# Optimization experiments

Hardware: AMD Instinct MI355X
Metric: run time of the kernel (lower is better)

## Reference

```python
import jax, jax.numpy as jnp
import numpy as np

D_MODEL = 768
NUM_HEADS = 12
D_K = D_MODEL // NUM_HEADS
D_FF = 3072
EPS = 1e-5


def _layer_norm(x, gamma, beta):
    mu = jnp.mean(x, axis=-1, keepdims=True)
    var = jnp.mean(jnp.square(x - mu), axis=-1, keepdims=True)
    return (x - mu) * jax.lax.rsqrt(var + EPS) * gamma + beta


def setup_inputs() -> dict:
    key = jax.random.key(0)
    ks = jax.random.split(key, 16)
    s = 1.0 / np.sqrt(D_MODEL)
    sf = 1.0 / np.sqrt(D_FF)
    inp = {
        "x": jax.random.normal(ks[0], (2, 2048, D_MODEL), dtype=jnp.float32),
        "Wq": jax.random.uniform(ks[1], (D_MODEL, D_MODEL), jnp.float32, -s, s),
        "bq": jax.random.uniform(ks[2], (D_MODEL,), jnp.float32, -s, s),
        "Wk": jax.random.uniform(ks[3], (D_MODEL, D_MODEL), jnp.float32, -s, s),
        "bk": jax.random.uniform(ks[4], (D_MODEL,), jnp.float32, -s, s),
        "Wv": jax.random.uniform(ks[5], (D_MODEL, D_MODEL), jnp.float32, -s, s),
        "bv": jax.random.uniform(ks[6], (D_MODEL,), jnp.float32, -s, s),
        "Wo": jax.random.uniform(ks[7], (D_MODEL, D_MODEL), jnp.float32, -s, s),
        "bo": jax.random.uniform(ks[8], (D_MODEL,), jnp.float32, -s, s),
        "W1": jax.random.uniform(ks[9], (D_MODEL, D_FF), jnp.float32, -s, s),
        "b1": jax.random.uniform(ks[10], (D_FF,), jnp.float32, -s, s),
        "W2": jax.random.uniform(ks[11], (D_FF, D_MODEL), jnp.float32, -sf, sf),
        "b2": jax.random.uniform(ks[12], (D_MODEL,), jnp.float32, -sf, sf),
        "g1": jnp.ones((D_MODEL,), jnp.float32),
        "be1": jnp.zeros((D_MODEL,), jnp.float32),
        "g2": jnp.ones((D_MODEL,), jnp.float32),
        "be2": jnp.zeros((D_MODEL,), jnp.float32),
    }
    return inp


def reference(x, Wq, bq, Wk, bk, Wv, bv, Wo, bo, W1, b1, W2, b2, g1, be1, g2, be2):
    B, S, _ = x.shape

    def split(h):  # (B,S,D) -> (B,H,S,Dk)
        return h.reshape(B, S, NUM_HEADS, D_K).transpose(0, 2, 1, 3)

    q = split(x @ Wq + bq)
    k = split(x @ Wk + bk)
    v = split(x @ Wv + bv)

    # naive attention: materialize full (B,H,S,S) scores as in the original
    scores = jnp.einsum("bhsd,bhtd->bhst", q, k) / np.sqrt(D_K)
    attn = jax.nn.softmax(scores, axis=-1)
    ctx = jnp.einsum("bhst,bhtd->bhsd", attn, v)
    ctx = ctx.transpose(0, 2, 1, 3).reshape(B, S, D_MODEL)
    attn_out = ctx @ Wo + bo

    x = _layer_norm(x + attn_out, g1, be1)
    ff = jax.nn.relu(x @ W1 + b1) @ W2 + b2
    x = _layer_norm(x + ff, g2, be2)
    return x
```

## Files before the change

kernel.cpp:

```cpp
#include <hip/hip_runtime.h>
#include <cstdint>


typedef unsigned short u16;
typedef unsigned int u32;
typedef __attribute__((ext_vector_type(4))) float f32x4;
typedef __attribute__((ext_vector_type(8))) short s16x8;
typedef __attribute__((ext_vector_type(4))) u16  u16x4;
typedef __attribute__((ext_vector_type(2))) u32  u32x2;

#define AS1 __attribute__((address_space(1)))
#define AS3 __attribute__((address_space(3)))

__device__ __forceinline__ u16 f2b(float f) {
  union { float f; unsigned u; } v; v.f = f;
  unsigned r = v.u + 0x7FFFu + ((v.u >> 16) & 1u);
  return (u16)(r >> 16);
}

__device__ __forceinline__ float b2f(u16 v) {
  union { float f; u32 u; } x; x.u = ((u32)v) << 16; return x.f;
}

__device__ __forceinline__ void gl_lds16(const void* g, void* lds_uniform_base) {
  __builtin_amdgcn_global_load_lds((const AS1 void*)g, (AS3 void*)lds_uniform_base, 16, 0, 0);
}

__device__ __forceinline__ f32x4 mfma16(s16x8 a, s16x8 b, f32x4 c) {
  return __builtin_amdgcn_mfma_f32_16x16x32_bf16(a, b, c, 0, 0, 0);
}

__device__ __forceinline__ u32 cvt_pk_bf16(float lo, float hi) {
  u32 r;
  asm("v_cvt_pk_bf16_f32 %0, %1, %2" : "=v"(r) : "v"(lo), "v"(hi));
  return r;
}

__device__ __forceinline__ float max3f(float a, float b, float c) {
  return fmaxf(fmaxf(a, b), c);
}

__device__ __forceinline__ void block_barrier() {
  asm volatile("" ::: "memory");
  __builtin_amdgcn_s_barrier();
  asm volatile("" ::: "memory");
}

__global__ __launch_bounds__(256) void prep(
    const float* __restrict__ Wq, const float* __restrict__ Wk,
    const float* __restrict__ Wv, const float* __restrict__ Wo,
    const float* __restrict__ W1, const float* __restrict__ W2,
    const float* __restrict__ bq, const float* __restrict__ bk,
    const float* __restrict__ bv, const float* __restrict__ x,
    u16* __restrict__ Wqkv_t, u16* __restrict__ Wo_t,
    u16* __restrict__ W1_t, u16* __restrict__ W2_t,
    float* __restrict__ bqkv, u16* __restrict__ Xb, int convBlocks) {
  __shared__ float ts[32][33];
  const int bid = blockIdx.x;
  const int tx = threadIdx.x, ty = threadIdx.y;
  if (bid < 6912) {
    const float* W; u16* Wt; int K, N, tile;
    if (bid < 2304) {
      int w = bid / 576; tile = bid - w * 576; K = 768; N = 768;
      W = (w == 0) ? Wq : (w == 1) ? Wk : (w == 2) ? Wv : Wo;
      Wt = (w < 3) ? Wqkv_t + (size_t)w * 768 * 768 : Wo_t;
    } else if (bid < 4608) {
      tile = bid - 2304; K = 768; N = 3072; W = W1; Wt = W1_t;
    } else {
      tile = bid - 4608; K = 3072; N = 768; W = W2; Wt = W2_t;
    }
    int ntx = N >> 5;
    int n0 = (tile % ntx) * 32, k0 = (tile / ntx) * 32;
#pragma unroll
    for (int yy = 0; yy < 32; yy += 8)
      ts[ty + yy][tx] = W[(size_t)(k0 + ty + yy) * N + n0 + tx];
    __syncthreads();
#pragma unroll
    for (int yy = 0; yy < 32; yy += 8)
      Wt[(size_t)(n0 + ty + yy) * K + k0 + tx] = f2b(ts[tx][ty + yy]);
  } else if (bid < 6912 + convBlocks) {
    int t = ty * 32 + tx;
    size_t i = ((size_t)(bid - 6912) * 256 + t) * 4;
    f32x4 v = *(const f32x4*)(x + i);
    u16x4 o;
#pragma unroll
    for (int k = 0; k < 4; ++k) o[k] = f2b(v[k]);
    *(u16x4*)(Xb + i) = o;
  } else {
    int t = ty * 32 + tx;
    int i = (bid - 6912 - convBlocks) * 256 + t;
    if (i < 2304) bqkv[i] = (i < 768) ? bq[i] : (i < 1536) ? bk[i - 768] : bv[i - 1536];
  }
}

template <int MODE>
__global__ __launch_bounds__(256) void gemm_bt(const u16* __restrict__ A,
                                               const u16* __restrict__ Bt,
                                               const float* __restrict__ bias,
                                               u16* __restrict__ Cb,
                                               u16* __restrict__ Qo, u16* __restrict__ Ko,
                                               u16* __restrict__ Vt, int M, int N, int K,
                                               int Klen) {
  __shared__ __align__(16) u16 lsA[2][128 * 64];
  __shared__ __align__(16) u16 lsB[2][128 * 64];
  const int tid = threadIdx.x;
  const int lane = tid & 63, wave = tid >> 6;
  const int lr = lane & 15, lh = lane >> 4;
  const int wr = wave >> 1, wc = wave & 1;

  int bx, by, bz;
  {
    int nx = gridDim.x, ny = gridDim.y, nz = gridDim.z;
    int total = nx * ny * nz;
    int lin = blockIdx.x + nx * (blockIdx.y + ny * blockIdx.z);
    if ((total & 7) == 0) {
      int key = (lin & 7) * (total >> 3) + (lin >> 3);
      by = key % ny;
      int t2 = key / ny;
      bz = t2 % nz;
      bx = t2 / nz;
    } else {
      bx = blockIdx.x; by = blockIdx.y; bz = blockIdx.z;
    }
  }
  const int m0 = by * 128;
  const int n0 = bx * 128;
  const int kB = bz * Klen;

  f32x4 acc[4][4];
#pragma unroll
  for (int i = 0; i < 4; ++i)
#pragma unroll
    for (int j = 0; j < 4; ++j) acc[i][j] = f32x4{0.f, 0.f, 0.f, 0.f};

  const size_t aBase = (size_t)m0 * K;
  const size_t bBase = (size_t)n0 * K;
  const int srow8 = tid >> 3;
  const int scolE = (((tid & 7) * 16) ^ ((srow8 & 7) << 4)) >> 1;
  const int xk = (lr & 7) << 4;

  auto stage = [&](int buf, int kt) {
#pragma unroll
    for (int i = 0; i < 4; ++i) {
      int row = i * 32 + srow8;
      int ldsOff = buf * 16384 + i * 4096 + wave * 1024;
      gl_lds16(A + aBase + (size_t)row * K + kt + scolE, (char*)lsA + ldsOff);
      gl_lds16(Bt + bBase + (size_t)row * K + kt + scolE, (char*)lsB + ldsOff);
    }
  };

  const int nk = Klen >> 6;
  stage(0, kB);
  for (int t = 0; t < nk; ++t) {
    const int cur = t & 1;
    if (t + 1 < nk) {
      stage(cur ^ 1, kB + (t + 1) * 64);
      asm volatile("s_waitcnt vmcnt(8)" ::: "memory");
    } else {
      asm volatile("s_waitcnt vmcnt(0)" ::: "memory");
    }
    block_barrier();
    const char* baA = (const char*)lsA + cur * 16384;
    const char* baB = (const char*)lsB + cur * 16384;
#pragma unroll
    for (int ks = 0; ks < 2; ++ks) {
      int cb = (ks * 64 + lh * 16) ^ xk;
      s16x8 a[4], b[4];
#pragma unroll
      for (int i = 0; i < 4; ++i) {
        a[i] = *(const s16x8*)(baA + (wr * 64 + i * 16 + lr) * 128 + cb);
        b[i] = *(const s16x8*)(baB + (wc * 64 + i * 16 + lr) * 128 + cb);
      }
#pragma unroll
      for (int i = 0; i < 4; ++i)
#pragma unroll
        for (int j = 0; j < 4; ++j) acc[i][j] = mfma16(a[i], b[j], acc[i][j]);
    }
    block_barrier();
  }

  u16* CbP = Cb + (size_t)bz * M * N;
#pragma unroll
  for (int i = 0; i < 4; ++i) {
    int growb = m0 + wr * 64 + i * 16 + lh * 4;
#pragma unroll
    for (int j = 0; j < 4; ++j) {
      int col = n0 + wc * 64 + j * 16 + lr;
      float bv = (MODE != 0 || bz == 0) ? bias[col] : 0.f;
      if (MODE == 2) {
        int sel = col / 768;
        int c2 = col - sel * 768;
        int h = c2 >> 6, d = c2 & 63;
        int b = growb >> 11, s0 = growb & 2047;
        if (sel == 2) {
          u16x4 ob;
#pragma unroll
          for (int q = 0; q < 4; ++q) ob[q] = f2b(acc[i][j][q] + bv);
          *(u16x4*)(Vt + (((size_t)(b * 12 + h)) * 64 + d) * 2048 + s0) = ob;
        } else {
#pragma unroll
          for (int q = 0; q < 4; ++q) {
            float v = acc[i][j][q] + bv;
            size_t idx = (((size_t)(b * 12 + h)) * 2048 + (s0 + q)) * 64 + d;
            float vv = (sel == 0) ? v * 0.1803368801f : v;
            u16* dst = (sel == 0) ? Qo : Ko;
            dst[idx] = f2b(vv);
          }
        }
      } else {
#pragma unroll
        for (int q = 0; q < 4; ++q) {
          int grow = growb + q;
          float v = acc[i][j][q] + bv;
          if (MODE == 0) {
            CbP[(size_t)grow * N + col] = f2b(v);
          } else {
            Cb[(size_t)grow * N + col] = f2b(fmaxf(v, 0.f));
          }
        }
      }
    }
  }
}

__global__ __launch_bounds__(512) void attn(const u16* __restrict__ Qh,
                                            const u16* __restrict__ Kh,
                                            const u16* __restrict__ Vt,
                                            u16* __restrict__ Opb,
                                            float* __restrict__ ml,
                                            int nbh, int ntile) {
  __shared__ __align__(16) u16 lsK[2][64 * 64];
  __shared__ __align__(16) u16 lsV[2][64 * 64];
  __shared__ __align__(16) u16 lsP[8][16 * 64];
  const int tid = threadIdx.x, lane = tid & 63, wave = tid >> 6;
  const int lr = lane & 15, lh = lane >> 4;

  int bx = blockIdx.x, bh = blockIdx.y, z = blockIdx.z;
  {
    int nz = gridDim.z;
    int total = 16 * nbh * nz;
    if ((total & 7) == 0) {
      int lin = bx + 16 * (bh + nbh * z);
      int nl = (lin & 7) * (total >> 3) + (lin >> 3);
      bx = nl & 15;
      bh = (nl >> 4) % nbh;
      z = nl / (16 * nbh);
    }
  }
  const int q0 = bx * 128 + wave * 16;
  const size_t kvBase = (size_t)bh * 2048 * 64;
  const int tB = z * ntile;

  const int srow = tid >> 3;
  const int scol = (((tid & 7) * 16) ^ ((srow & 7) << 4)) >> 1;
  const u16* kSrcBase = Kh + kvBase + (size_t)srow * 64 + scol;
  const u16* vSrcBase = Vt + kvBase + (size_t)srow * 2048 + scol;

  s16x8 qf[2];
#pragma unroll
  for (int ks = 0; ks < 2; ++ks)
    qf[ks] = *(const s16x8*)(Qh + kvBase + (size_t)(q0 + lr) * 64 + ks * 32 + lh * 8);

  s16x8 onesf;
#pragma unroll
  for (int k = 0; k < 8; ++k) onesf[k] = (short)0x3F80;

  f32x4 oacc[4];
  f32x4 aOnes = f32x4{0.f, 0.f, 0.f, 0.f};
  float mrow = -1e30f;
#pragma unroll
  for (int d = 0; d < 4; ++d) oacc[d] = f32x4{0.f, 0.f, 0.f, 0.f};

  gl_lds16(kSrcBase + (size_t)tB * 4096, (char*)lsK[0] + wave * 1024);
  gl_lds16(vSrcBase + tB * 64,           (char*)lsV[0] + wave * 1024);

  for (int it = 0; it < ntile; ++it) {
    const int cur = it & 1;
    __syncthreads();

    s16x8 kb[2][4];
#pragma unroll
    for (int ks = 0; ks < 2; ++ks)
#pragma unroll
      for (int j = 0; j < 4; ++j) {
        int r = j * 16 + lr;
        kb[ks][j] = *(const s16x8*)((const char*)lsK[cur] + r * 128 +
                                    ((ks * 64 + lh * 16) ^ ((r & 7) << 4)));
      }

    if (it + 1 < ntile) {
      int t = tB + it + 1;
      gl_lds16(kSrcBase + (size_t)t * 4096, (char*)lsK[cur ^ 1] + wave * 1024);
      gl_lds16(vSrcBase + t * 64,           (char*)lsV[cur ^ 1] + wave * 1024);
    }

    f32x4 st[4];
#pragma unroll
    for (int j = 0; j < 4; ++j) st[j] = f32x4{0.f, 0.f, 0.f, 0.f};
    __builtin_amdgcn_s_setprio(1);
#pragma unroll
    for (int ks = 0; ks < 2; ++ks)
#pragma unroll
      for (int j = 0; j < 4; ++j) st[j] = mfma16(kb[ks][j], qf[ks], st[j]);
    __builtin_amdgcn_s_setprio(0);

    float mx;
    {
      float t0 = max3f(st[0][0], st[0][1], st[0][2]);
      float t1 = max3f(st[0][3], st[1][0], st[1][1]);
      float t2 = max3f(st[1][2], st[1][3], st[2][0]);
      float t3 = max3f(st[2][1], st[2][2], st[2][3]);
      float t4 = max3f(st[3][0], st[3][1], st[3][2]);
      mx = fmaxf(max3f(t0, t1, t2), max3f(t3, t4, st[3][3]));
      mx = fmaxf(mx, __shfl_xor(mx, 16));
      mx = fmaxf(mx, __shfl_xor(mx, 32));
    }
    if (__any(mx > mrow + 11.f)) {
      float mn = fmaxf(mrow, mx);
      float al = exp2f(mrow - mn);
      mrow = mn;
#pragma unroll
      for (int q = 0; q < 4; ++q) aOnes[q] *= al;
#pragma unroll
      for (int d = 0; d < 4; ++d)
#pragma unroll
        for (int q = 0; q < 4; ++q) oacc[d][q] *= al;
    }

#pragma unroll
    for (int j = 0; j < 4; ++j) {
      float p0 = exp2f(st[j][0] - mrow);
      float p1 = exp2f(st[j][1] - mrow);
      float p2 = exp2f(st[j][2] - mrow);
      float p3 = exp2f(st[j][3] - mrow);
      u32x2 pk;
      pk.x = cvt_pk_bf16(p0, p1);
      pk.y = cvt_pk_bf16(p2, p3);
      *(u32x2*)((char*)lsP[wave] + lr * 128 + ((j * 32 + lh * 8) ^ ((lr & 7) << 4))) = pk;
    }

    __builtin_amdgcn_s_setprio(1);
#pragma unroll
    for (int ks = 0; ks < 2; ++ks) {
      s16x8 pa = *(const s16x8*)((const char*)lsP[wave] + lr * 128 +
                                 ((ks * 64 + lh * 16) ^ ((lr & 7) << 4)));
      aOnes = mfma16(onesf, pa, aOnes);
#pragma unroll
      for (int d = 0; d < 4; ++d) {
        int r = d * 16 + lr;
        s16x8 vb = *(const s16x8*)((const char*)lsV[cur] + r * 128 +
                                   ((ks * 64 + lh * 16) ^ ((r & 7) << 4)));
        oacc[d] = mfma16(vb, pa, oacc[d]);
      }
    }
    __builtin_amdgcn_s_setprio(0);
  }

  {
    int s = q0 + lr;
    size_t r = ((size_t)z * nbh + bh) * 2048 + s;
#pragma unroll
    for (int d = 0; d < 4; ++d) {
      u32x2 pk;
      pk.x = cvt_pk_bf16(oacc[d][0], oacc[d][1]);
      pk.y = cvt_pk_bf16(oacc[d][2], oacc[d][3]);
      *(u32x2*)(Opb + r * 64 + d * 16 + lh * 4) = pk;
    }
    if (lh == 0) { ml[r * 2] = mrow; ml[r * 2 + 1] = aOnes[0]; }
  }
}

template <int NZ>
__global__ __launch_bounds__(256) void attn_combine(const u16* __restrict__ Opb,
                                                    const float* __restrict__ ml,
                                                    u16* __restrict__ ctx, int nbh) {
  size_t i = (size_t)blockIdx.x * 256 + threadIdx.x;
  int d4 = (int)(i & 15);
  size_t rs = i >> 4;
  size_t zs = (size_t)nbh * 2048;
  float m[NZ], l[NZ];
  float mx = -1e30f;
#pragma unroll
  for (int p = 0; p < NZ; ++p) {
    m[p] = ml[(p * zs + rs) * 2];
    l[p] = ml[(p * zs + rs) * 2 + 1];
    mx = fmaxf(mx, m[p]);
  }
  float wsum = 0.f, a[NZ];
#pragma unroll
  for (int p = 0; p < NZ; ++p) { a[p] = exp2f(m[p] - mx); wsum += l[p] * a[p]; }
  float inv = 1.f / wsum;
  f32x4 o = f32x4{0.f, 0.f, 0.f, 0.f};
#pragma unroll
  for (int p = 0; p < NZ; ++p) {
    u16x4 op = *(const u16x4*)(Opb + (p * zs + rs) * 64 + d4 * 4);
#pragma unroll
    for (int k = 0; k < 4; ++k) o[k] += b2f(op[k]) * a[p];
  }
  int bh = (int)(rs >> 11), s = (int)(rs & 2047);
  int b = bh / 12, h = bh - b * 12;
  u16x4 r;
#pragma unroll
  for (int k = 0; k < 4; ++k) r[k] = f2b(o[k] * inv);
  *(u16x4*)(ctx + ((size_t)(b * 2048 + s)) * 768 + h * 64 + d4 * 4) = r;
}

template <int NP>
__global__ __launch_bounds__(256) void resid_ln(const float* __restrict__ xin,
                                                const u16* __restrict__ yp,
                                                size_t pstride,
                                                const float* __restrict__ gamma,
                                                const float* __restrict__ beta,
                                                float* __restrict__ outf,
                                                u16* __restrict__ outb) {
  const int row = blockIdx.x, t = threadIdx.x;
  const size_t base4 = (size_t)row * 192;
  const bool act = t < 192;
  f32x4 v = f32x4{0.f, 0.f, 0.f, 0.f};
  float s = 0.f, s2 = 0.f;
  if (act) {
    v = ((const f32x4*)xin)[base4 + t];
#pragma unroll
    for (int p = 0; p < NP; ++p) {
      u16x4 y = *(const u16x4*)(yp + p * pstride + (size_t)row * 768 + t * 4);
#pragma unroll
      for (int k = 0; k < 4; ++k) v[k] += b2f(y[k]);
    }
    s = (v[0] + v[1]) + (v[2] + v[3]);
    s2 = (v[0] * v[0] + v[1] * v[1]) + (v[2] * v[2] + v[3] * v[3]);
  }
#pragma unroll
  for (int off = 32; off > 0; off >>= 1) {
    s += __shfl_down(s, off, 64);
    s2 += __shfl_down(s2, off, 64);
  }
  __shared__ float red[8];
  int lane = t & 63, wave = t >> 6;
  if (lane == 0) { red[wave] = s; red[4 + wave] = s2; }
  __syncthreads();
  s = red[0] + red[1] + red[2] + red[3];
  s2 = red[4] + red[5] + red[6] + red[7];
  const float inv = 1.f / 768.f;
  float mu = s * inv;
  float var = fmaxf(s2 * inv - mu * mu, 0.f);
  float rs = rsqrtf(var + 1e-5f);
  if (act) {
    f32x4 g = ((const f32x4*)gamma)[t];
    f32x4 bb = ((const f32x4*)beta)[t];
    f32x4 o;
#pragma unroll
    for (int k = 0; k < 4; ++k) o[k] = (v[k] - mu) * rs * g[k] + bb[k];
    if (outf) ((f32x4*)outf)[base4 + t] = o;
    if (outb) {
      u16x4 ob;
#pragma unroll
      for (int k = 0; k < 4; ++k) ob[k] = f2b(o[k]);
      ((u16x4*)outb)[base4 + t] = ob;
    }
  }
}

extern "C" void kernel_launch(void* const* d_in, const int* in_sizes, int n_in,
                              void* d_out, int out_size, void* d_ws, size_t ws_size,
                              hipStream_t stream) {
  const float* x   = (const float*)d_in[0];
  const float* Wq  = (const float*)d_in[1];
  const float* bq  = (const float*)d_in[2];
  const float* Wk  = (const float*)d_in[3];
  const float* bk  = (const float*)d_in[4];
  const float* Wv  = (const float*)d_in[5];
  const float* bv  = (const float*)d_in[6];
  const float* Wo  = (const float*)d_in[7];
  const float* bo  = (const float*)d_in[8];
  const float* W1  = (const float*)d_in[9];
  const float* b1  = (const float*)d_in[10];
  const float* W2  = (const float*)d_in[11];
  const float* b2  = (const float*)d_in[12];
  const float* g1  = (const float*)d_in[13];
  const float* be1 = (const float*)d_in[14];
  const float* g2  = (const float*)d_in[15];
  const float* be2 = (const float*)d_in[16];
  float* out = (float*)d_out;

  const int M = in_sizes[0] / 768;
  const int B = M / 2048;
  const int nbh = B * 12;

  char* ws = (char*)d_ws;
  size_t off = 0;
  auto alloc = [&](size_t bytes) -> void* {
    void* p = ws + off;
    off += (bytes + 255) & ~(size_t)255;
    return p;
  };
  u16*   Wqkv_t = (u16*)alloc((size_t)2304 * 768 * 2);
  u16*   Wo_t   = (u16*)alloc((size_t)768 * 768 * 2);
  u16*   W1_t   = (u16*)alloc((size_t)3072 * 768 * 2);
  u16*   W2_t   = (u16*)alloc((size_t)768 * 3072 * 2);
  float* bqkv   = (float*)alloc(2304 * 4);
  u16*   Xb     = (u16*)alloc((size_t)M * 768 * 2);
  u16*   Qh     = (u16*)alloc((size_t)M * 768 * 2);
  u16*   Kh     = (u16*)alloc((size_t)M * 768 * 2);
  u16*   Vt     = (u16*)alloc((size_t)M * 768 * 2);

  size_t pstride = (size_t)M * 768;
  size_t fixedRest = pstride * 4  + pstride * 2  +
                     (size_t)M * 3072 * 2  + 4096;
  const int ZSPLIT = 2;
  size_t opElems = (size_t)ZSPLIT * nbh * 2048 * 64;
  size_t attnBytes = opElems * 2 + (size_t)ZSPLIT * nbh * 2048 * 2 * 4;
  size_t reg4 = attnBytes;
  if (reg4 < pstride * 2 * 4) reg4 = pstride * 2 * 4;
  int FSPLIT;
  size_t regionBytes;
  if (off + reg4 + fixedRest <= ws_size) {
    FSPLIT = 4; regionBytes = reg4;
  } else {
    FSPLIT = 2;
    regionBytes = attnBytes > pstride * 2 * 2 ? attnBytes : pstride * 2 * 2;
  }
  float* region = (float*)alloc(regionBytes);
  u16*   Opb  = (u16*)region;
  float* ml   = (float*)((char*)region + opElems * 2);
  u16*   projPart = (u16*)region;
  u16*   ffnPart  = (u16*)region;
  float* x1f  = (float*)alloc(pstride * 4);
  u16*   x1b  = (u16*)alloc(pstride * 2);
  u16*   hb   = (u16*)alloc((size_t)M * 3072 * 2);
  u16*   ctx  = Xb;

  dim3 tb(32, 8);
  const int convBlocks = (M * 768) / 1024;
  prep<<<6912 + convBlocks + 9, tb, 0, stream>>>(
      Wq, Wk, Wv, Wo, W1, W2, bq, bk, bv, x,
      Wqkv_t, Wo_t, W1_t, W2_t, bqkv, Xb, convBlocks);

  gemm_bt<2><<<dim3(2304 / 128, M / 128), 256, 0, stream>>>(
      Xb, Wqkv_t, bqkv, nullptr, Qh, Kh, Vt, M, 2304, 768, 768);

  attn<<<dim3(16, nbh, ZSPLIT), 512, 0, stream>>>(Qh, Kh, Vt, Opb, ml, nbh, 32 / ZSPLIT);
  attn_combine<2><<<nbh * 128, 256, 0, stream>>>(Opb, ml, ctx, nbh);

  gemm_bt<0><<<dim3(768 / 128, M / 128, 2), 256, 0, stream>>>(
      ctx, Wo_t, bo, projPart, nullptr, nullptr, nullptr, M, 768, 768, 384);

  resid_ln<2><<<M, 256, 0, stream>>>(x, projPart, pstride, g1, be1, x1f, x1b);

  gemm_bt<1><<<dim3(3072 / 128, M / 128), 256, 0, stream>>>(
      x1b, W1_t, b1, hb, nullptr, nullptr, nullptr, M, 3072, 768, 768);

  if (FSPLIT == 4) {
    gemm_bt<0><<<dim3(768 / 128, M / 128, 4), 256, 0, stream>>>(
        hb, W2_t, b2, ffnPart, nullptr, nullptr, nullptr, M, 768, 3072, 768);
    resid_ln<4><<<M, 256, 0, stream>>>(x1f, ffnPart, pstride, g2, be2, out, nullptr);
  } else {
    gemm_bt<0><<<dim3(768 / 128, M / 128, 2), 256, 0, stream>>>(
        hb, W2_t, b2, ffnPart, nullptr, nullptr, nullptr, M, 768, 3072, 1536);
    resid_ln<2><<<M, 256, 0, stream>>>(x1f, ffnPart, pstride, g2, be2, out, nullptr);
  }
}
```

Measured before the change: 202.5 us.

## Single-buffer attention K/V via register prefetch and fold max subtraction into MFMA init

Replaces the double-buffered direct global-to-LDS K/V loads with a register-staged prefetch into a single LDS buffer, which halves K/V shared memory but adds a second barrier per tile. The running max is now subtracted by seeding the score accumulators with -mrow, so the exp no longer needs a per-element subtraction except on rescale tiles. This aims to raise occupancy and remove VALU subtractions, at the cost of extra register pressure and synchronisation.

New measurement: 210.2 us. 1.04x slower.

```diff
diff --git a/kernel.cpp b/kernel.cpp
--- a/kernel.cpp
+++ b/kernel.cpp
@@ -229,8 +229,8 @@
                                             u16* __restrict__ Opb,
                                             float* __restrict__ ml,
                                             int nbh, int ntile) {
-  __shared__ __align__(16) u16 lsK[2][64 * 64];
-  __shared__ __align__(16) u16 lsV[2][64 * 64];
+  __shared__ __align__(16) u16 lsK[64 * 64];
+  __shared__ __align__(16) u16 lsV[64 * 64];
   __shared__ __align__(16) u16 lsP[8][16 * 64];
   const int tid = threadIdx.x, lane = tid & 63, wave = tid >> 6;
   const int lr = lane & 15, lh = lane >> 4;
@@ -267,16 +267,23 @@
 
   f32x4 oacc[4];
   f32x4 aOnes = f32x4{0.f, 0.f, 0.f, 0.f};
-  float mrow = -1e30f;
+  float mrow = 0.f;
 #pragma unroll
   for (int d = 0; d < 4; ++d) oacc[d] = f32x4{0.f, 0.f, 0.f, 0.f};
 
-  gl_lds16(kSrcBase + (size_t)tB * 4096, (char*)lsK[0] + wave * 1024);
-  gl_lds16(vSrcBase + tB * 64,           (char*)lsV[0] + wave * 1024);
+  s16x8 kr = *(const s16x8*)(kSrcBase + (size_t)tB * 4096);
+  s16x8 vr = *(const s16x8*)(vSrcBase + tB * 64);
+  *(s16x8*)((char*)lsK + tid * 16) = kr;
+  *(s16x8*)((char*)lsV + tid * 16) = vr;
+  __syncthreads();
 
   for (int it = 0; it < ntile; ++it) {
-    const int cur = it & 1;
-    __syncthreads();
+    const bool more = (it + 1 < ntile);
+    if (more) {
+      int t = tB + it + 1;
+      kr = *(const s16x8*)(kSrcBase + (size_t)t * 4096);
+      vr = *(const s16x8*)(vSrcBase + t * 64);
+    }
 
     s16x8 kb[2][4];
 #pragma unroll
@@ -284,19 +291,14 @@
 #pragma unroll
       for (int j = 0; j < 4; ++j) {
         int r = j * 16 + lr;
-        kb[ks][j] = *(const s16x8*)((const char*)lsK[cur] + r * 128 +
+        kb[ks][j] = *(const s16x8*)((const char*)lsK + r * 128 +
                                     ((ks * 64 + lh * 16) ^ ((r & 7) << 4)));
       }
 
-    if (it + 1 < ntile) {
-      int t = tB + it + 1;
-      gl_lds16(kSrcBase + (size_t)t * 4096, (char*)lsK[cur ^ 1] + wave * 1024);
-      gl_lds16(vSrcBase + t * 64,           (char*)lsV[cur ^ 1] + wave * 1024);
-    }
-
+    const float negm = -mrow;
     f32x4 st[4];
 #pragma unroll
-    for (int j = 0; j < 4; ++j) st[j] = f32x4{0.f, 0.f, 0.f, 0.f};
+    for (int j = 0; j < 4; ++j) st[j] = f32x4{negm, negm, negm, negm};
     __builtin_amdgcn_s_setprio(1);
 #pragma unroll
     for (int ks = 0; ks < 2; ++ks)
@@ -315,10 +317,10 @@
       mx = fmaxf(mx, __shfl_xor(mx, 16));
       mx = fmaxf(mx, __shfl_xor(mx, 32));
     }
-    if (__any(mx > mrow + 11.f)) {
-      float mn = fmaxf(mrow, mx);
-      float al = exp2f(mrow - mn);
-      mrow = mn;
+    const bool resc = __any(mx > 11.f);
+    if (resc) {
+      float al = exp2f(-mx);
+      mrow += mx;
 #pragma unroll
       for (int q = 0; q < 4; ++q) aOnes[q] *= al;
 #pragma unroll
@@ -327,16 +329,30 @@
         for (int q = 0; q < 4; ++q) oacc[d][q] *= al;
     }
 
-#pragma unroll
-    for (int j = 0; j < 4; ++j) {
-      float p0 = exp2f(st[j][0] - mrow);
-      float p1 = exp2f(st[j][1] - mrow);
-      float p2 = exp2f(st[j][2] - mrow);
-      float p3 = exp2f(st[j][3] - mrow);
-      u32x2 pk;
-      pk.x = cvt_pk_bf16(p0, p1);
-      pk.y = cvt_pk_bf16(p2, p3);
-      *(u32x2*)((char*)lsP[wave] + lr * 128 + ((j * 32 + lh * 8) ^ ((lr & 7) << 4))) = pk;
+    if (resc) {
+#pragma unroll
+      for (int j = 0; j < 4; ++j) {
+        float p0 = exp2f(st[j][0] - mx);
+        float p1 = exp2f(st[j][1] - mx);
+        float p2 = exp2f(st[j][2] - mx);
+        float p3 = exp2f(st[j][3] - mx);
+        u32x2 pk;
+        pk.x = cvt_pk_bf16(p0, p1);
+        pk.y = cvt_pk_bf16(p2, p3);
+        *(u32x2*)((char*)lsP[wave] + lr * 128 + ((j * 32 + lh * 8) ^ ((lr & 7) << 4))) = pk;
+      }
+    } else {
+#pragma unroll
+      for (int j = 0; j < 4; ++j) {
+        float p0 = exp2f(st[j][0]);
+        float p1 = exp2f(st[j][1]);
+        float p2 = exp2f(st[j][2]);
+        float p3 = exp2f(st[j][3]);
+        u32x2 pk;
+        pk.x = cvt_pk_bf16(p0, p1);
+        pk.y = cvt_pk_bf16(p2, p3);
+        *(u32x2*)((char*)lsP[wave] + lr * 128 + ((j * 32 + lh * 8) ^ ((lr & 7) << 4))) = pk;
+      }
     }
 
     __builtin_amdgcn_s_setprio(1);
@@ -348,12 +364,19 @@
 #pragma unroll
       for (int d = 0; d < 4; ++d) {
         int r = d * 16 + lr;
-        s16x8 vb = *(const s16x8*)((const char*)lsV[cur] + r * 128 +
+        s16x8 vb = *(const s16x8*)((const char*)lsV + r * 128 +
                                    ((ks * 64 + lh * 16) ^ ((r & 7) << 4)));
         oacc[d] = mfma16(vb, pa, oacc[d]);
       }
     }
     __builtin_amdgcn_s_setprio(0);
+
+    __syncthreads();
+    if (more) {
+      *(s16x8*)((char*)lsK + tid * 16) = kr;
+      *(s16x8*)((char*)lsV + tid * 16) = vr;
+      __syncthreads();
+    }
   }
 
   {
```
